# Performance work log

Hardware: AMD Instinct MI355X
Metric: run time of the kernel (lower is better)

The kernel has to match this reference:

```python
import jax, jax.numpy as jnp
import numpy as np

WS = 16; HEADS = 6; TOPK = 64; KIN = 128; EPS = 1e-10
B, C, H, W = 1, 192, 192, 192
HID = 4 * C  # mlp_ratio * dim


def _ln(x, g, b):
    m = jnp.mean(x, axis=-1, keepdims=True)
    v = jnp.var(x, axis=-1, keepdims=True)
    return (x - m) * jax.lax.rsqrt(v + 1e-5) * g + b


def _dw_gelu(x, hw, w, b):
    # depthwise 5x5 conv + exact GELU on token sequence (B, N, C)
    Bx, N, Cx = x.shape
    h, wd = hw
    xi = x.transpose(0, 2, 1).reshape(Bx, Cx, h, wd)
    y = jax.lax.conv_general_dilated(xi, w, (1, 1), 'SAME',
        feature_group_count=Cx, dimension_numbers=('NCHW', 'OIHW', 'NCHW'))
    y = jax.nn.gelu(y + b[None, :, None, None], approximate=False)
    return y.reshape(Bx, Cx, N).transpose(0, 2, 1)


def _window_partition(x):
    b, h, w, c = x.shape
    x = x.reshape(b, h // WS, WS, w // WS, WS, c)
    return x.transpose(0, 1, 3, 2, 4, 5).reshape(-1, WS * WS, c)


def _window_reverse(win, h, w):
    c = win.shape[-1]
    b = win.shape[0] // ((h // WS) * (w // WS))
    x = win.reshape(b, h // WS, w // WS, WS, WS, c)
    return x.transpose(0, 1, 3, 2, 4, 5).reshape(b, h, w, c)


def setup_inputs():
    key = jax.random.key(0)
    ks = jax.random.split(key, 16)
    b_, n = B * (H // WS) * (W // WS), WS * WS
    wgen = lambda k, sh: jax.random.normal(k, sh, jnp.float32) * 0.02
    p = {}
    p['features_mv'] = jax.random.normal(ks[0], (B, C, H, W), jnp.float32)
    p['pfa_values'] = jax.random.uniform(ks[1], (b_, HEADS, n, KIN), jnp.float32)
    p['pfa_indices'] = jax.random.randint(ks[2], (b_, HEADS, n, KIN), 0, n, jnp.int32)
    p['rpi'] = jax.random.randint(ks[3], (n, n), 0, (2 * WS - 1) ** 2, jnp.int32)
    p['ln1_g'] = jnp.ones((C,)); p['ln1_b'] = jnp.zeros((C,))
    p['Wq_w'] = wgen(ks[4], (C, C)); p['Wq_b'] = jnp.zeros((C,))
    p['Wk_w'] = wgen(ks[5], (C, C)); p['Wk_b'] = jnp.zeros((C,))
    p['Wv_w'] = wgen(ks[6], (C, C)); p['Wv_b'] = jnp.zeros((C,))
    p['lepe_w'] = wgen(ks[7], (C, 1, 5, 5)); p['lepe_b'] = jnp.zeros((C,))
    p['rpb_table'] = wgen(ks[8], ((2 * WS - 1) ** 2, HEADS))
    p['proj_w'] = wgen(ks[9], (C, C)); p['proj_b'] = jnp.zeros((C,))
    p['ln2_g'] = jnp.ones((C,)); p['ln2_b'] = jnp.zeros((C,))
    p['fc1_w'] = wgen(ks[10], (C, HID)); p['fc1_b'] = jnp.zeros((HID,))
    p['ffn_dw_w'] = wgen(ks[11], (HID, 1, 5, 5)); p['ffn_dw_b'] = jnp.zeros((HID,))
    p['fc2_w'] = wgen(ks[12], (HID, C)); p['fc2_b'] = jnp.zeros((C,))
    return p


def reference(features_mv, pfa_values, pfa_indices, rpi, ln1_g, ln1_b,
              Wq_w, Wq_b, Wk_w, Wk_b, Wv_w, Wv_b, lepe_w, lepe_b, rpb_table,
              proj_w, proj_b, ln2_g, ln2_b, fc1_w, fc1_b, ffn_dw_w, ffn_dw_b,
              fc2_w, fc2_b):
    b, c, h, w = features_mv.shape
    hd = c // HEADS
    x = features_mv.reshape(b, c, h * w).transpose(0, 2, 1)  # (B, HW, C)
    shortcut = x
    xn = _ln(x, ln1_g, ln1_b)
    q = xn @ Wq_w + Wq_b
    k = xn @ Wk_w + Wk_b
    v = xn @ Wv_w + Wv_b
    vl = _dw_gelu(v, (h, w), lepe_w, lepe_b)  # v_LePE
    qkvp = jnp.concatenate([q, k, v, vl], axis=-1).reshape(b, h, w, 4 * c)
    xw = _window_partition(qkvp)  # (b_, n, 4C)
    b_, n = xw.shape[0], WS * WS
    qkvp = xw.reshape(b_, n, 4, HEADS, hd).transpose(2, 0, 3, 1, 4)
    q, k, v, vl = qkvp[0] * hd ** -0.5, qkvp[1], qkvp[2], qkvp[3]
    # SMM_QmK: per-query gathered q.k — dense scores then index gather
    scores = jnp.einsum('bhid,bhjd->bhij', q, k)          # (b_, H, n, n)
    attn = jnp.take_along_axis(scores, pfa_indices, axis=-1)  # (b_, H, n, K)
    # relative position bias, gathered by the same sparse indices
    rpb = rpb_table[rpi.reshape(-1)].reshape(n, n, HEADS).transpose(2, 0, 1)
    rpb_g = jnp.take_along_axis(jnp.broadcast_to(rpb[None], (b_, HEADS, n, n)),
                                pfa_indices, axis=-1)
    attn = jax.nn.softmax(attn + rpb_g, axis=-1)
    # progressive focused attention: multiply by prior values, renormalize
    attn = attn * pfa_values
    attn = (attn + EPS) / (jnp.sum(attn, axis=-1, keepdims=True) + EPS)
    # in-layer top-k reselection (topk=64 < KIN=128)
    tv, ti = jax.lax.top_k(attn, TOPK)
    idx = jnp.take_along_axis(pfa_indices, ti, axis=-1)   # (b_, H, n, TOPK)
    # SMM_AmV: scatter sparse attn to dense (duplicates sum) then matmul
    BH = b_ * HEADS
    a = tv.reshape(BH, n, TOPK)
    idxf = idx.reshape(BH, n, TOPK)
    dense = jnp.zeros((BH, n, n), tv.dtype).at[
        jnp.arange(BH)[:, None, None], jnp.arange(n)[None, :, None], idxf].add(a)
    xo = jnp.einsum('bij,bjd->bid', dense, v.reshape(BH, n, hd))
    xo = xo.reshape(b_, HEADS, n, hd) + vl
    xo = xo.transpose(0, 2, 1, 3).reshape(b_, n, c) @ proj_w + proj_b
    xr = _window_reverse(xo.reshape(-1, WS, WS, c), h, w)
    x = shortcut + xr.reshape(b, h * w, c)
    # ConvFFN
    y = _ln(x, ln2_g, ln2_b) @ fc1_w + fc1_b
    y = jax.nn.gelu(y, approximate=False)
    y = y + _dw_gelu(y, (h, w), ffn_dw_w, ffn_dw_b)
    x = x + (y @ fc2_w + fc2_b)
    return x
```

## Files before the change

kernel.cpp:

```cpp
#include <hip/hip_runtime.h>
#include <math.h>

#define HW 36864
#define CD 192
#define NH 6
#define HDIM 32
#define HIDD 768

typedef unsigned short u16;
typedef __attribute__((ext_vector_type(8))) short bf16x8;
typedef __attribute__((ext_vector_type(4))) float f32x4;

__device__ __forceinline__ float gelu_f(float x) {
  return 0.5f * x * (1.0f + erff(x * 0.70710678118654752f));
}
__device__ __forceinline__ u16 f2b(float f) {
  union { float f; unsigned u; } v; v.f = f;
  unsigned r = v.u + 0x7fff + ((v.u >> 16) & 1);
  return (u16)(r >> 16);
}
__device__ __forceinline__ float b2f(u16 b) {
  union { unsigned u; float f; } v; v.u = ((unsigned)b) << 16;
  return v.f;
}
__device__ __forceinline__ float ldv(const float* p) { return *p; }
__device__ __forceinline__ float ldv(const u16* p) { return b2f(*p); }

__global__ __launch_bounds__(256)
void lnt_kernel(const float* __restrict__ in, const float* __restrict__ g,
                const float* __restrict__ b, u16* __restrict__ outTM)
{
  __shared__ float tile[64][193];
  __shared__ float red[64][8];
  __shared__ float2 stat2[64];
  __shared__ float gb[384];
  const int tid = threadIdx.x;
  const int part = tid >> 6, tk = tid & 63;
  const int tok = blockIdx.x * 64 + tk;
  if (tid < 192) { gb[tid] = g[tid]; gb[192 + tid] = b[tid]; }
  float s = 0.f, sq = 0.f;
  for (int c = part * 48; c < part * 48 + 48; ++c) {
    float v = in[(size_t)c * HW + tok];
    tile[tk][c] = v; s += v; sq += v * v;
  }
  red[tk][part] = s; red[tk][4 + part] = sq;
  __syncthreads();
  if (tid < 64) {
    float ss = red[tid][0] + red[tid][1] + red[tid][2] + red[tid][3];
    float qq = red[tid][4] + red[tid][5] + red[tid][6] + red[tid][7];
    float m = ss * (1.0f / CD);
    float var = fmaxf(qq * (1.0f / CD) - m * m, 0.f);
    stat2[tid] = make_float2(m, rsqrtf(var + 1e-5f));
  }
  __syncthreads();
  unsigned* op = (unsigned*)outTM + (size_t)blockIdx.x * 6144;
  #pragma unroll
  for (int r = 0; r < 24; ++r) {
    int idx = tid + r * 256;
    int tok2 = idx / 96, dc = idx - tok2 * 96;
    float2 st = stat2[tok2];
    int c = dc * 2;
    float v0 = (tile[tok2][c] - st.x) * st.y * gb[c] + gb[192 + c];
    float v1 = (tile[tok2][c + 1] - st.x) * st.y * gb[c + 1] + gb[192 + c + 1];
    op[idx] = (unsigned)f2b(v0) | ((unsigned)f2b(v1) << 16);
  }
}

__global__ __launch_bounds__(256)
void trans_kernel(const u16* __restrict__ in, u16* __restrict__ out, int C)
{
  __shared__ u16 ls[64][34];
  const int m0 = blockIdx.x * 64, c0 = blockIdx.y * 32;
  const int t = threadIdx.x;
  #pragma unroll
  for (int r = 0; r < 4; ++r) {
    int idx = t + r * 256;
    int c = idx >> 5, dm = idx & 31;
    unsigned d = *(const unsigned*)(in + (size_t)(c0 + c) * HW + m0 + dm * 2);
    ls[dm * 2][c] = (u16)d;
    ls[dm * 2 + 1][c] = (u16)(d >> 16);
  }
  __syncthreads();
  #pragma unroll
  for (int r = 0; r < 4; ++r) {
    int idx = t + r * 256;
    int m = idx >> 4, dc = idx & 15;
    unsigned d = (unsigned)ls[m][dc * 2] | ((unsigned)ls[m][dc * 2 + 1] << 16);
    *(unsigned*)(out + (size_t)(m0 + m) * C + c0 + dc * 2) = d;
  }
}

__global__ __launch_bounds__(256)
void wtrans_kernel(const float* __restrict__ in, u16* __restrict__ out, int K, int N)
{
  __shared__ float ls[32][33];
  const int k0 = blockIdx.x * 32, n0 = blockIdx.y * 32;
  const int t = threadIdx.x;
  #pragma unroll
  for (int r = 0; r < 4; ++r) {
    int idx = t + r * 256;
    int k = idx >> 5, n = idx & 31;
    ls[k][n] = in[(size_t)(k0 + k) * N + n0 + n];
  }
  __syncthreads();
  #pragma unroll
  for (int r = 0; r < 4; ++r) {
    int idx = t + r * 256;
    int n = idx >> 5, k = idx & 31;
    out[(size_t)(n0 + n) * K + k0 + k] = f2b(ls[k][n]);
  }
}

__global__ __launch_bounds__(256)
void wtrans4_kernel(const float* __restrict__ w0, const float* __restrict__ w1,
                    const float* __restrict__ w2, const float* __restrict__ w3,
                    u16* __restrict__ out)
{
  __shared__ float ls[32][33];
  const int z = blockIdx.z;
  const float* in = (z == 0) ? w0 : (z == 1 ? w1 : (z == 2 ? w2 : w3));
  u16* op = out + (size_t)z * CD * CD;
  const int k0 = blockIdx.x * 32, n0 = blockIdx.y * 32;
  const int t = threadIdx.x;
  #pragma unroll
  for (int r = 0; r < 4; ++r) {
    int idx = t + r * 256;
    int k = idx >> 5, n = idx & 31;
    ls[k][n] = in[(size_t)(k0 + k) * CD + n0 + n];
  }
  __syncthreads();
  #pragma unroll
  for (int r = 0; r < 4; ++r) {
    int idx = t + r * 256;
    int n = idx >> 5, k = idx & 31;
    op[(size_t)(n0 + n) * CD + k0 + k] = f2b(ls[k][n]);
  }
}

template<int MODE>
__global__ __launch_bounds__(256, 4)
void mgemm_kernel(const u16* __restrict__ A,
                  const u16* __restrict__ W0, const u16* __restrict__ W1, const u16* __restrict__ W2,
                  const float* __restrict__ b0, const float* __restrict__ b1, const float* __restrict__ b2,
                  const float* __restrict__ aux, void* __restrict__ outv,
                  int K, int segN)
{
  const int n0 = blockIdx.x * 64;
  const int m0 = blockIdx.y * 128;
  const int seg = n0 / segN;
  const u16* Wp = (seg == 0) ? W0 : (seg == 1 ? W1 : W2);
  const float* biasp = (seg == 0) ? b0 : (seg == 1 ? b1 : b2);
  const int nl0 = n0 - seg * segN;

  __shared__ u16 As[128 * 32];
  __shared__ u16 Bs[64 * 32];

  const int tid = threadIdx.x;
  const int lane = tid & 63, wave = tid >> 6;
  const int wm = (wave >> 1) * 64, wn = (wave & 1) * 32;
  const int fm = lane & 15, fq = lane >> 4;
  const int ar = tid >> 2, akq = tid & 3;

  f32x4 acc[4][2];
  #pragma unroll
  for (int i = 0; i < 4; ++i) { acc[i][0] = (f32x4)(0.f); acc[i][1] = (f32x4)(0.f); }

  uint4 rA0, rA1, rB, nA0, nA1, nB;
  rA0 = *(const uint4*)(A + (size_t)(m0 + ar) * K + akq * 8);
  rA1 = *(const uint4*)(A + (size_t)(m0 + ar + 64) * K + akq * 8);
  rB  = *(const uint4*)(Wp + (size_t)(nl0 + ar) * K + akq * 8);

  for (int k0 = 0; k0 < K; k0 += 32) {
    *(uint4*)(&As[ar * 32 + akq * 8]) = rA0;
    *(uint4*)(&As[(ar + 64) * 32 + akq * 8]) = rA1;
    *(uint4*)(&Bs[ar * 32 + akq * 8]) = rB;
    __syncthreads();
    const int kn = (k0 + 32 < K) ? k0 + 32 : k0;
    nA0 = *(const uint4*)(A + (size_t)(m0 + ar) * K + kn + akq * 8);
    nA1 = *(const uint4*)(A + (size_t)(m0 + ar + 64) * K + kn + akq * 8);
    nB  = *(const uint4*)(Wp + (size_t)(nl0 + ar) * K + kn + akq * 8);
    bf16x8 af[4], bf[2];
    #pragma unroll
    for (int mt = 0; mt < 4; ++mt)
      af[mt] = *(const bf16x8*)(&As[(wm + mt * 16 + fm) * 32 + fq * 8]);
    #pragma unroll
    for (int nt = 0; nt < 2; ++nt)
      bf[nt] = *(const bf16x8*)(&Bs[(wn + nt * 16 + fm) * 32 + fq * 8]);
    #pragma unroll
    for (int mt = 0; mt < 4; ++mt)
      #pragma unroll
      for (int nt = 0; nt < 2; ++nt)
        acc[mt][nt] = __builtin_amdgcn_mfma_f32_16x16x32_bf16(af[mt], bf[nt], acc[mt][nt], 0, 0, 0);
    __syncthreads();
    rA0 = nA0; rA1 = nA1; rB = nB;
  }

  #pragma unroll
  for (int nt = 0; nt < 2; ++nt) {
    const int n = n0 + wn + nt * 16 + fm;
    const float bia = biasp[nl0 + wn + nt * 16 + fm];
    #pragma unroll
    for (int mt = 0; mt < 4; ++mt) {
      const int mb = m0 + wm + mt * 16 + fq * 4;
      float o[4];
      #pragma unroll
      for (int r = 0; r < 4; ++r) o[r] = acc[mt][nt][r] + bia;
      if (MODE == 0) {
        const float sc = (seg == 0) ? 0.17677669529663689f : 1.0f;
        u16 h0 = f2b(o[0] * sc), h1 = f2b(o[1] * sc), h2 = f2b(o[2] * sc), h3 = f2b(o[3] * sc);
        uint2 pk = make_uint2((unsigned)h0 | ((unsigned)h1 << 16), (unsigned)h2 | ((unsigned)h3 << 16));
        *(uint2*)((u16*)outv + (size_t)n * HW + mb) = pk;
      } else if (MODE == 1) {
        const float4 ax = *(const float4*)(aux + (size_t)n * HW + mb);
        *(float4*)((float*)outv + (size_t)n * HW + mb) =
            make_float4(o[0] + ax.x, o[1] + ax.y, o[2] + ax.z, o[3] + ax.w);
      } else if (MODE == 2) {
        u16 h0 = f2b(gelu_f(o[0])), h1 = f2b(gelu_f(o[1]));
        u16 h2 = f2b(gelu_f(o[2])), h3 = f2b(gelu_f(o[3]));
        uint2 pk = make_uint2((unsigned)h0 | ((unsigned)h1 << 16), (unsigned)h2 | ((unsigned)h3 << 16));
        *(uint2*)((u16*)outv + (size_t)n * HW + mb) = pk;
      } else {
        const float4 ax = *(const float4*)(aux + (size_t)n * HW + mb);
        float* op = (float*)outv;
        op[(size_t)(mb + 0) * CD + n] = o[0] + ax.x;
        op[(size_t)(mb + 1) * CD + n] = o[1] + ax.y;
        op[(size_t)(mb + 2) * CD + n] = o[2] + ax.z;
        op[(size_t)(mb + 3) * CD + n] = o[3] + ax.w;
      }
    }
  }
}

template<bool ADD>
__global__ __launch_bounds__(256)
void dwconv_kernel(const u16* __restrict__ in, const float* __restrict__ w,
                   const float* __restrict__ bias, u16* __restrict__ out)
{
  const int plane = blockIdx.z;
  const int bx = blockIdx.x * 64, by = blockIdx.y * 4;
  __shared__ float tile[8][68];
  __shared__ float ws[26];
  const int tid = threadIdx.x;
  if (tid < 26) ws[tid] = (tid < 25) ? w[plane * 25 + tid] : bias[plane];
  const u16* ip = in + (size_t)plane * HW;
  for (int e = tid; e < 544; e += 256) {
    int r = e / 68, cc = e - r * 68;
    int gy = by + r - 2, gx = bx + cc - 2;
    tile[r][cc] = (gy >= 0 && gy < 192 && gx >= 0 && gx < 192) ? b2f(ip[gy * 192 + gx]) : 0.f;
  }
  __syncthreads();
  const int tx = tid & 63, ty = tid >> 6;
  float acc = 0.f;
  #pragma unroll
  for (int dy = 0; dy < 5; ++dy)
    #pragma unroll
    for (int dx = 0; dx < 5; ++dx)
      acc = fmaf(tile[ty + dy][tx + dx], ws[dy * 5 + dx], acc);
  float v = gelu_f(acc + ws[25]);
  if (ADD) v += tile[ty + 2][tx + 2];
  out[(size_t)plane * HW + (by + ty) * 192 + bx + tx] = f2b(v);
}

__global__ __launch_bounds__(512, 4)
void attn_kernel(const u16* __restrict__ qg, const u16* __restrict__ kg,
                 const u16* __restrict__ vg, const u16* __restrict__ vlg,
                 const float* __restrict__ pfa_v, const int* __restrict__ pfa_i,
                 const int* __restrict__ rpi, const float* __restrict__ rpb_t,
                 u16* __restrict__ attn_out)
{
  const int h = blockIdx.x;
  const int win = blockIdx.y;
  const int wy = (win / 12) * 16;
  const int wx = (win - (win / 12) * 12) * 16;
  const size_t hb = (size_t)h * HDIM * HW;

  __shared__ u16 kT[256][40];
  __shared__ u16 vT[32][258];
  __shared__ float Sb[32][264];
  __shared__ u16 qT[32][40];
  __shared__ float rpb_h[964];
  __shared__ float2 selbuf[8][64];

  const int tid = threadIdx.x;
  const int lane = tid & 63, wave = tid >> 6;

  for (int r = tid; r < 961; r += 512) rpb_h[r] = rpb_t[r * 6 + h];

  #pragma unroll
  for (int r = 0; r < 8; ++r) {
    int idx = tid + r * 512;
    int d = idx >> 7, jp = idx & 127, j = jp * 2;
    int pg = (wy + (j >> 4)) * 192 + (wx + (j & 15));
    ushort2 kv = *(const ushort2*)(kg + hb + (size_t)d * HW + pg);
    kT[j][d] = kv.x; kT[j + 1][d] = kv.y;
    *(ushort2*)&vT[d][j] = *(const ushort2*)(vg + hb + (size_t)d * HW + pg);
  }
  __syncthreads();

  const size_t wb = ((size_t)win * NH + h) * 256;

  for (int pass = 0; pass < 8; ++pass) {
    {
      int d = tid >> 4, ip = tid & 15, i = pass * 32 + ip * 2;
      int pg = (wy + (i >> 4)) * 192 + (wx + (i & 15));
      ushort2 qv = *(const ushort2*)(qg + hb + (size_t)d * HW + pg);
      qT[ip * 2][d] = qv.x; qT[ip * 2 + 1][d] = qv.y;
    }
    __syncthreads();
    {
      const int it = wave & 1;
      bf16x8 aq = *(const bf16x8*)&qT[it * 16 + (lane & 15)][(lane >> 4) * 8];
      #pragma unroll
      for (int t = 0; t < 4; ++t) {
        int j0 = ((wave >> 1) * 4 + t) * 16;
        bf16x8 bk = *(const bf16x8*)&kT[j0 + (lane & 15)][(lane >> 4) * 8];
        f32x4 c = __builtin_amdgcn_mfma_f32_16x16x32_bf16(aq, bk, (f32x4)(0.f), 0, 0, 0);
        const int col = j0 + (lane & 15), rowb = it * 16 + (lane >> 4) * 4;
        Sb[rowb + 0][col] = c[0]; Sb[rowb + 1][col] = c[1];
        Sb[rowb + 2][col] = c[2]; Sb[rowb + 3][col] = c[3];
      }
    }
    __syncthreads();
    int pj1[4], pj2[4]; float pv1[4], pv2[4], rb1[4], rb2[4];
    #pragma unroll
    for (int u = 0; u < 4; ++u) {
      const int i = pass * 32 + u * 8 + wave;
      const size_t base = (wb + (size_t)i) * 128;
      pj1[u] = pfa_i[base + lane];  pj2[u] = pfa_i[base + 64 + lane];
      pv1[u] = pfa_v[base + lane];  pv2[u] = pfa_v[base + 64 + lane];
    }
    #pragma unroll
    for (int u = 0; u < 4; ++u) {
      const int i = pass * 32 + u * 8 + wave;
      rb1[u] = rpb_h[rpi[i * 256 + pj1[u]]];
      rb2[u] = rpb_h[rpi[i * 256 + pj2[u]]];
    }
    #pragma unroll
    for (int u = 0; u < 4; ++u) {
      const int iq = u * 8 + wave;
      const int i  = pass * 32 + iq;
      const int j1 = pj1[u], j2 = pj2[u];
      float s1 = Sb[iq][j1] + rb1[u];
      float s2 = Sb[iq][j2] + rb2[u];
      float mx = fmaxf(s1, s2);
      #pragma unroll
      for (int o = 32; o > 0; o >>= 1) mx = fmaxf(mx, __shfl_xor(mx, o));
      float e1 = expf(s1 - mx), e2 = expf(s2 - mx);
      float sA = e1 + e2;
      float sB = e1 * pv1[u] + e2 * pv2[u];
      #pragma unroll
      for (int o = 32; o > 0; o >>= 1) { sA += __shfl_xor(sA, o); sB += __shfl_xor(sB, o); }
      const float rs = 1.0f / sA;
      float a1 = e1 * rs * pv1[u];
      float a2 = e2 * rs * pv2[u];
      const float rden = 1.0f / (sB * rs + 1e-10f);
      a1 = (a1 + 1e-10f) * rden;
      a2 = (a2 + 1e-10f) * rden;
      const unsigned ub1 = __float_as_uint(a1), ub2 = __float_as_uint(a2);
      unsigned thr = 0u;
      for (int bit = 30; bit >= 0; --bit) {
        unsigned cand = thr | (1u << bit);
        int cnt = (int)__popcll(__ballot(ub1 >= cand)) + (int)__popcll(__ballot(ub2 >= cand));
        if (cnt >= 64) { thr = cand; if (cnt == 64) break; }
      }
      const unsigned long long lmlt = (1ull << lane) - 1ull;
      const bool gt1 = ub1 > thr, gt2 = ub2 > thr;
      const bool eq1 = ub1 == thr, eq2 = ub2 == thr;
      const unsigned long long meq1 = __ballot(eq1), meq2 = __ballot(eq2);
      const int need = 64 - (int)__popcll(__ballot(gt1)) - (int)__popcll(__ballot(gt2));
      const bool sel1 = gt1 || (eq1 && (int)__popcll(meq1 & lmlt) < need);
      const bool sel2 = gt2 || (eq2 && ((int)__popcll(meq1) + (int)__popcll(meq2 & lmlt)) < need);
      const unsigned long long ms1 = __ballot(sel1), ms2 = __ballot(sel2);
      const int pos1 = (int)__popcll(ms1 & lmlt);
      const int pos2 = (int)__popcll(ms1) + (int)__popcll(ms2 & lmlt);
      if (sel1) selbuf[wave][pos1] = make_float2(a1, __int_as_float(j1));
      if (sel2) selbuf[wave][pos2] = make_float2(a2, __int_as_float(j2));
      const int d = lane & 31, half = lane >> 5;
      float acc = 0.f;
      #pragma unroll
      for (int c = 0; c < 4; ++c) {
        float2 sv[8];
        #pragma unroll
        for (int q4 = 0; q4 < 4; ++q4)
          *(float4*)&sv[q4 * 2] = *(const float4*)&selbuf[wave][half * 32 + c * 8 + q4 * 2];
        #pragma unroll
        for (int s = 0; s < 8; ++s)
          acc = fmaf(sv[s].x, b2f(vT[d][__float_as_int(sv[s].y)]), acc);
      }
      acc += __shfl_xor(acc, 32);
      const int pg = (wy + (i >> 4)) * 192 + (wx + (i & 15));
      if (lane < 32) {
        float o = acc + b2f(vlg[hb + (size_t)d * HW + pg]);
        attn_out[(size_t)pg * CD + h * HDIM + d] = f2b(o);
      }
    }
    __syncthreads();
  }
}

extern "C" void kernel_launch(void* const* d_in, const int* in_sizes, int n_in,
                              void* d_out, int out_size, void* d_ws, size_t ws_size,
                              hipStream_t stream)
{
  (void)in_sizes; (void)n_in; (void)out_size; (void)ws_size;
  const float* features = (const float*)d_in[0];
  const float* pfa_v    = (const float*)d_in[1];
  const int*   pfa_i    = (const int*)d_in[2];
  const int*   rpi      = (const int*)d_in[3];
  const float* ln1_g    = (const float*)d_in[4];
  const float* ln1_b    = (const float*)d_in[5];
  const float* Wq_w     = (const float*)d_in[6];
  const float* Wq_b     = (const float*)d_in[7];
  const float* Wk_w     = (const float*)d_in[8];
  const float* Wk_b     = (const float*)d_in[9];
  const float* Wv_w     = (const float*)d_in[10];
  const float* Wv_b     = (const float*)d_in[11];
  const float* lepe_w   = (const float*)d_in[12];
  const float* lepe_b   = (const float*)d_in[13];
  const float* rpb_t    = (const float*)d_in[14];
  const float* proj_w   = (const float*)d_in[15];
  const float* proj_b   = (const float*)d_in[16];
  const float* ln2_g    = (const float*)d_in[17];
  const float* ln2_b    = (const float*)d_in[18];
  const float* fc1_w    = (const float*)d_in[19];
  const float* fc1_b    = (const float*)d_in[20];
  const float* dw_w     = (const float*)d_in[21];
  const float* dw_b     = (const float*)d_in[22];
  const float* fc2_w    = (const float*)d_in[23];
  const float* fc2_b    = (const float*)d_in[24];

  char* ws = (char*)d_ws;
  const size_t S  = (size_t)HW * CD;
  const size_t SB = S * 4;
  u16*   xnt    = (u16*)(ws);
  u16*   qkvb   = (u16*)(ws + SB / 2);
  u16*   q_ = qkvb; u16* k_ = qkvb + S; u16* v_ = qkvb + 2 * S;
  u16*   vl     = (u16*)(ws + 2 * SB);
  u16*   attn_o = (u16*)(ws + 2 * SB + SB / 2);
  float* x2     = (float*)(ws + 3 * SB);
  u16*   xn2t   = (u16*)(ws + 4 * SB);
  u16*   y_     = (u16*)(ws + 4 * SB + SB / 2);
  u16*   y2_    = (u16*)(ws + 6 * SB + SB / 2);
  u16*   y2t    = (u16*)(ws);
  u16*   wqt  = (u16*)(ws + 8 * SB + SB / 2);
  u16*   wkt  = wqt + 36864;
  u16*   wvt  = wkt + 36864;
  u16*   wpt  = wvt + 36864;
  u16*   wf1t = wpt + 36864;
  u16*   wf2t = wf1t + 147456;
  float* out = (float*)d_out;

  wtrans4_kernel<<<dim3(6, 6, 4), 256, 0, stream>>>(Wq_w, Wk_w, Wv_w, proj_w, wqt);
  wtrans_kernel<<<dim3(6, 24), 256, 0, stream>>>(fc1_w, wf1t, 192, 768);
  wtrans_kernel<<<dim3(24, 6), 256, 0, stream>>>(fc2_w, wf2t, 768, 192);
  lnt_kernel<<<dim3(HW / 64), 256, 0, stream>>>(features, ln1_g, ln1_b, xnt);
  mgemm_kernel<0><<<dim3(9, HW / 128), 256, 0, stream>>>(xnt, wqt, wkt, wvt, Wq_b, Wk_b, Wv_b,
                                                         nullptr, qkvb, 192, 192);
  dwconv_kernel<false><<<dim3(3, 48, 192), 256, 0, stream>>>(v_, lepe_w, lepe_b, vl);
  attn_kernel<<<dim3(6, 144), 512, 0, stream>>>(q_, k_, v_, vl, pfa_v, pfa_i, rpi, rpb_t, attn_o);
  mgemm_kernel<1><<<dim3(3, HW / 128), 256, 0, stream>>>(attn_o, wpt, wpt, wpt, proj_b, proj_b, proj_b,
                                                         features, x2, 192, 1 << 30);
  lnt_kernel<<<dim3(HW / 64), 256, 0, stream>>>(x2, ln2_g, ln2_b, xn2t);
  mgemm_kernel<2><<<dim3(12, HW / 128), 256, 0, stream>>>(xn2t, wf1t, wf1t, wf1t, fc1_b, fc1_b, fc1_b,
                                                          nullptr, y_, 192, 1 << 30);
  dwconv_kernel<true><<<dim3(3, 48, 768), 256, 0, stream>>>(y_, dw_w, dw_b, y2_);
  trans_kernel<<<dim3(HW / 64, 24), 256, 0, stream>>>(y2_, y2t, HIDD);
  mgemm_kernel<3><<<dim3(3, HW / 128), 256, 0, stream>>>(y2t, wf2t, wf2t, wf2t, fc2_b, fc2_b, fc2_b,
                                                         x2, out, 768, 1 << 30);
}
```

Before: 800.7 us.

## Fuse dwconv with transpose, precompute dense RPB, pad GEMM LDS, simplify attention normalization

The depthwise conv kernel now processes 32 channels per block and writes token-major output directly, so the separate transpose kernel goes away and the attention reads LEPE token-major. A new kernel expands the relative position bias into a dense per-head 256x256 table once. The attention adds that bias straight after the MFMA instead of doing gathered rpi lookups, and moves the softmax/renormalisation algebra after top-k so fewer values are rescaled. GEMM shared-memory tiles are padded from 32 to 40 columns to reduce bank conflicts. The cost is an extra 1.5 MB bias table read per window-head and a larger LDS footprint in the conv kernel.

```diff
diff --git a/kernel.cpp b/kernel.cpp
--- a/kernel.cpp
+++ b/kernel.cpp
@@ -23,8 +23,12 @@
   union { unsigned u; float f; } v; v.u = ((unsigned)b) << 16;
   return v.f;
 }
-__device__ __forceinline__ float ldv(const float* p) { return *p; }
-__device__ __forceinline__ float ldv(const u16* p) { return b2f(*p); }
+__device__ __forceinline__ float b2f_lo(unsigned u) {
+  union { unsigned x; float f; } v; v.x = u << 16; return v.f;
+}
+__device__ __forceinline__ float b2f_hi(unsigned u) {
+  union { unsigned x; float f; } v; v.x = u & 0xffff0000u; return v.f;
+}
 
 __global__ __launch_bounds__(256)
 void lnt_kernel(const float* __restrict__ in, const float* __restrict__ g,
@@ -67,30 +71,6 @@
 }
 
 __global__ __launch_bounds__(256)
-void trans_kernel(const u16* __restrict__ in, u16* __restrict__ out, int C)
-{
-  __shared__ u16 ls[64][34];
-  const int m0 = blockIdx.x * 64, c0 = blockIdx.y * 32;
-  const int t = threadIdx.x;
-  #pragma unroll
-  for (int r = 0; r < 4; ++r) {
-    int idx = t + r * 256;
-    int c = idx >> 5, dm = idx & 31;
-    unsigned d = *(const unsigned*)(in + (size_t)(c0 + c) * HW + m0 + dm * 2);
-    ls[dm * 2][c] = (u16)d;
-    ls[dm * 2 + 1][c] = (u16)(d >> 16);
-  }
-  __syncthreads();
-  #pragma unroll
-  for (int r = 0; r < 4; ++r) {
-    int idx = t + r * 256;
-    int m = idx >> 4, dc = idx & 15;
-    unsigned d = (unsigned)ls[m][dc * 2] | ((unsigned)ls[m][dc * 2 + 1] << 16);
-    *(unsigned*)(out + (size_t)(m0 + m) * C + c0 + dc * 2) = d;
-  }
-}
-
-__global__ __launch_bounds__(256)
 void wtrans_kernel(const float* __restrict__ in, u16* __restrict__ out, int K, int N)
 {
   __shared__ float ls[32][33];
@@ -135,6 +115,17 @@
     int n = idx >> 5, k = idx & 31;
     op[(size_t)(n0 + n) * CD + k0 + k] = f2b(ls[k][n]);
   }
+}
+
+__global__ __launch_bounds__(256)
+void rpbg_kernel(const int* __restrict__ rpi, const float* __restrict__ rpb_t,
+                 float* __restrict__ out)
+{
+  const int i = blockIdx.x, j = threadIdx.x;
+  const int r = rpi[i * 256 + j];
+  #pragma unroll
+  for (int h = 0; h < NH; ++h)
+    out[(size_t)h * 65536 + i * 256 + j] = rpb_t[r * NH + h];
 }
 
 template<int MODE>
@@ -152,8 +143,8 @@
   const float* biasp = (seg == 0) ? b0 : (seg == 1 ? b1 : b2);
   const int nl0 = n0 - seg * segN;
 
-  __shared__ u16 As[128 * 32];
-  __shared__ u16 Bs[64 * 32];
+  __shared__ u16 As[128 * 40];
+  __shared__ u16 Bs[64 * 40];
 
   const int tid = threadIdx.x;
   const int lane = tid & 63, wave = tid >> 6;
@@ -171,9 +162,9 @@
   rB  = *(const uint4*)(Wp + (size_t)(nl0 + ar) * K + akq * 8);
 
   for (int k0 = 0; k0 < K; k0 += 32) {
-    *(uint4*)(&As[ar * 32 + akq * 8]) = rA0;
-    *(uint4*)(&As[(ar + 64) * 32 + akq * 8]) = rA1;
-    *(uint4*)(&Bs[ar * 32 + akq * 8]) = rB;
+    *(uint4*)(&As[ar * 40 + akq * 8]) = rA0;
+    *(uint4*)(&As[(ar + 64) * 40 + akq * 8]) = rA1;
+    *(uint4*)(&Bs[ar * 40 + akq * 8]) = rB;
     __syncthreads();
     const int kn = (k0 + 32 < K) ? k0 + 32 : k0;
     nA0 = *(const uint4*)(A + (size_t)(m0 + ar) * K + kn + akq * 8);
@@ -182,10 +173,10 @@
     bf16x8 af[4], bf[2];
     #pragma unroll
     for (int mt = 0; mt < 4; ++mt)
-      af[mt] = *(const bf16x8*)(&As[(wm + mt * 16 + fm) * 32 + fq * 8]);
+      af[mt] = *(const bf16x8*)(&As[(wm + mt * 16 + fm) * 40 + fq * 8]);
     #pragma unroll
     for (int nt = 0; nt < 2; ++nt)
-      bf[nt] = *(const bf16x8*)(&Bs[(wn + nt * 16 + fm) * 32 + fq * 8]);
+      bf[nt] = *(const bf16x8*)(&Bs[(wn + nt * 16 + fm) * 40 + fq * 8]);
     #pragma unroll
     for (int mt = 0; mt < 4; ++mt)
       #pragma unroll
@@ -233,40 +224,82 @@
 
 template<bool ADD>
 __global__ __launch_bounds__(256)
-void dwconv_kernel(const u16* __restrict__ in, const float* __restrict__ w,
-                   const float* __restrict__ bias, u16* __restrict__ out)
-{
-  const int plane = blockIdx.z;
+void dwconv_tm_kernel(const u16* __restrict__ in, const float* __restrict__ w,
+                      const float* __restrict__ bias, u16* __restrict__ out, int PL)
+{
+  const int p0 = blockIdx.z * 32;
   const int bx = blockIdx.x * 64, by = blockIdx.y * 4;
-  __shared__ float tile[8][68];
-  __shared__ float ws[26];
+  __shared__ u16 tile[32 * 546];
+  __shared__ float ws[32][26];
   const int tid = threadIdx.x;
-  if (tid < 26) ws[tid] = (tid < 25) ? w[plane * 25 + tid] : bias[plane];
-  const u16* ip = in + (size_t)plane * HW;
-  for (int e = tid; e < 544; e += 256) {
-    int r = e / 68, cc = e - r * 68;
-    int gy = by + r - 2, gx = bx + cc - 2;
-    tile[r][cc] = (gy >= 0 && gy < 192 && gx >= 0 && gx < 192) ? b2f(ip[gy * 192 + gx]) : 0.f;
-  }
-  __syncthreads();
-  const int tx = tid & 63, ty = tid >> 6;
-  float acc = 0.f;
-  #pragma unroll
-  for (int dy = 0; dy < 5; ++dy)
-    #pragma unroll
-    for (int dx = 0; dx < 5; ++dx)
-      acc = fmaf(tile[ty + dy][tx + dx], ws[dy * 5 + dx], acc);
-  float v = gelu_f(acc + ws[25]);
-  if (ADD) v += tile[ty + 2][tx + 2];
-  out[(size_t)plane * HW + (by + ty) * 192 + bx + tx] = f2b(v);
+  for (int e = tid; e < 832; e += 256) {
+    int p = e / 26, q = e - p * 26;
+    ws[p][q] = (q < 25) ? w[(p0 + p) * 25 + q] : bias[p0 + p];
+  }
+  for (int e = tid; e < 256 * 34; e += 256) {
+    int rp = e / 34, ch = e - rp * 34;
+    int p = rp >> 3, r = rp & 7;
+    int gy = by + r - 2, gx = bx + ch * 2 - 2;
+    unsigned val = 0;
+    if (gy >= 0 && gy < 192 && gx >= 0 && gx < 192)
+      val = *(const unsigned*)(in + (size_t)(p0 + p) * HW + gy * 192 + gx);
+    *(unsigned*)&tile[p * 546 + r * 68 + ch * 2] = val;
+  }
+  __syncthreads();
+  const int txp = tid >> 3, pg = tid & 7;
+  u16 res[4][2][4];
+  #pragma unroll
+  for (int pp = 0; pp < 4; ++pp) {
+    const int p = pg * 4 + pp;
+    const u16* tp = &tile[p * 546];
+    float o0[4] = {0.f, 0.f, 0.f, 0.f}, o1[4] = {0.f, 0.f, 0.f, 0.f};
+    #pragma unroll
+    for (int ir = 0; ir < 8; ++ir) {
+      const unsigned* rowp = (const unsigned*)(tp + ir * 68 + txp * 2);
+      unsigned ua = rowp[0], ub = rowp[1], uc = rowp[2];
+      float f0 = b2f_lo(ua), f1 = b2f_hi(ua), f2 = b2f_lo(ub);
+      float f3 = b2f_hi(ub), f4 = b2f_lo(uc), f5 = b2f_hi(uc);
+      #pragma unroll
+      for (int dy = 0; dy < 5; ++dy) {
+        const int r = ir - dy;
+        if (r >= 0 && r < 4) {
+          const float w0 = ws[p][dy * 5 + 0], w1 = ws[p][dy * 5 + 1], w2 = ws[p][dy * 5 + 2];
+          const float w3 = ws[p][dy * 5 + 3], w4 = ws[p][dy * 5 + 4];
+          o0[r] += f0 * w0 + f1 * w1 + f2 * w2 + f3 * w3 + f4 * w4;
+          o1[r] += f1 * w0 + f2 * w1 + f3 * w2 + f4 * w3 + f5 * w4;
+        }
+      }
+    }
+    const float bb = ws[p][25];
+    #pragma unroll
+    for (int r = 0; r < 4; ++r) {
+      float v0 = gelu_f(o0[r] + bb);
+      float v1 = gelu_f(o1[r] + bb);
+      if (ADD) {
+        unsigned ctr = *(const unsigned*)(tp + (r + 2) * 68 + txp * 2 + 2);
+        v0 += b2f_lo(ctr); v1 += b2f_hi(ctr);
+      }
+      res[pp][0][r] = f2b(v0); res[pp][1][r] = f2b(v1);
+    }
+  }
+  #pragma unroll
+  for (int r = 0; r < 4; ++r) {
+    #pragma unroll
+    for (int c = 0; c < 2; ++c) {
+      const int pix = (by + r) * 192 + bx + txp * 2 + c;
+      uint2 pk = make_uint2(
+        (unsigned)res[0][c][r] | ((unsigned)res[1][c][r] << 16),
+        (unsigned)res[2][c][r] | ((unsigned)res[3][c][r] << 16));
+      *(uint2*)(out + (size_t)pix * PL + p0 + pg * 4) = pk;
+    }
+  }
 }
 
 __global__ __launch_bounds__(512, 4)
 void attn_kernel(const u16* __restrict__ qg, const u16* __restrict__ kg,
-                 const u16* __restrict__ vg, const u16* __restrict__ vlg,
+                 const u16* __restrict__ vg, const u16* __restrict__ vlt,
                  const float* __restrict__ pfa_v, const int* __restrict__ pfa_i,
-                 const int* __restrict__ rpi, const float* __restrict__ rpb_t,
-                 u16* __restrict__ attn_out)
+                 const float* __restrict__ rpbg, u16* __restrict__ attn_out)
 {
   const int h = blockIdx.x;
   const int win = blockIdx.y;
@@ -274,17 +307,14 @@
   const int wx = (win - (win / 12) * 12) * 16;
   const size_t hb = (size_t)h * HDIM * HW;
 
-  __shared__ u16 kT[256][40];
-  __shared__ u16 vT[32][258];
-  __shared__ float Sb[32][264];
-  __shared__ u16 qT[32][40];
-  __shared__ float rpb_h[964];
+  __shared__ u16 kT[256 * 40];
+  __shared__ u16 vJ[256 * 40];
+  __shared__ float Sb[32 * 260];
+  __shared__ u16 qT[32 * 40];
   __shared__ float2 selbuf[8][64];
 
   const int tid = threadIdx.x;
   const int lane = tid & 63, wave = tid >> 6;
-
-  for (int r = tid; r < 961; r += 512) rpb_h[r] = rpb_t[r * 6 + h];
 
   #pragma unroll
   for (int r = 0; r < 8; ++r) {
@@ -292,36 +322,44 @@
     int d = idx >> 7, jp = idx & 127, j = jp * 2;
     int pg = (wy + (j >> 4)) * 192 + (wx + (j & 15));
     ushort2 kv = *(const ushort2*)(kg + hb + (size_t)d * HW + pg);
-    kT[j][d] = kv.x; kT[j + 1][d] = kv.y;
-    *(ushort2*)&vT[d][j] = *(const ushort2*)(vg + hb + (size_t)d * HW + pg);
+    kT[j * 40 + d] = kv.x; kT[(j + 1) * 40 + d] = kv.y;
+    ushort2 vv = *(const ushort2*)(vg + hb + (size_t)d * HW + pg);
+    vJ[j * 40 + d] = vv.x; vJ[(j + 1) * 40 + d] = vv.y;
   }
   __syncthreads();
 
   const size_t wb = ((size_t)win * NH + h) * 256;
+  const float* rpp = rpbg + (size_t)h * 65536;
 
   for (int pass = 0; pass < 8; ++pass) {
     {
       int d = tid >> 4, ip = tid & 15, i = pass * 32 + ip * 2;
       int pg = (wy + (i >> 4)) * 192 + (wx + (i & 15));
       ushort2 qv = *(const ushort2*)(qg + hb + (size_t)d * HW + pg);
-      qT[ip * 2][d] = qv.x; qT[ip * 2 + 1][d] = qv.y;
+      qT[(ip * 2) * 40 + d] = qv.x; qT[(ip * 2 + 1) * 40 + d] = qv.y;
     }
     __syncthreads();
     {
       const int it = wave & 1;
-      bf16x8 aq = *(const bf16x8*)&qT[it * 16 + (lane & 15)][(lane >> 4) * 8];
+      const int fm = lane & 15, fq = lane >> 4;
+      bf16x8 aq = *(const bf16x8*)&qT[(it * 16 + fm) * 40 + fq * 8];
       #pragma unroll
       for (int t = 0; t < 4; ++t) {
         int j0 = ((wave >> 1) * 4 + t) * 16;
-        bf16x8 bk = *(const bf16x8*)&kT[j0 + (lane & 15)][(lane >> 4) * 8];
+        bf16x8 bk = *(const bf16x8*)&kT[(j0 + fm) * 40 + fq * 8];
         f32x4 c = __builtin_amdgcn_mfma_f32_16x16x32_bf16(aq, bk, (f32x4)(0.f), 0, 0, 0);
-        const int col = j0 + (lane & 15), rowb = it * 16 + (lane >> 4) * 4;
-        Sb[rowb + 0][col] = c[0]; Sb[rowb + 1][col] = c[1];
-        Sb[rowb + 2][col] = c[2]; Sb[rowb + 3][col] = c[3];
+        const int col = j0 + fm, rowb = it * 16 + fq * 4;
+        const int ib = pass * 32 + rowb;
+        c[0] += rpp[(size_t)(ib + 0) * 256 + col];
+        c[1] += rpp[(size_t)(ib + 1) * 256 + col];
+        c[2] += rpp[(size_t)(ib + 2) * 256 + col];
+        c[3] += rpp[(size_t)(ib + 3) * 256 + col];
+        Sb[(rowb + 0) * 260 + col] = c[0]; Sb[(rowb + 1) * 260 + col] = c[1];
+        Sb[(rowb + 2) * 260 + col] = c[2]; Sb[(rowb + 3) * 260 + col] = c[3];
       }
     }
     __syncthreads();
-    int pj1[4], pj2[4]; float pv1[4], pv2[4], rb1[4], rb2[4];
+    int pj1[4], pj2[4]; float pv1[4], pv2[4];
     #pragma unroll
     for (int u = 0; u < 4; ++u) {
       const int i = pass * 32 + u * 8 + wave;
@@ -331,38 +369,26 @@
     }
     #pragma unroll
     for (int u = 0; u < 4; ++u) {
-      const int i = pass * 32 + u * 8 + wave;
-      rb1[u] = rpb_h[rpi[i * 256 + pj1[u]]];
-      rb2[u] = rpb_h[rpi[i * 256 + pj2[u]]];
-    }
-    #pragma unroll
-    for (int u = 0; u < 4; ++u) {
       const int iq = u * 8 + wave;
       const int i  = pass * 32 + iq;
       const int j1 = pj1[u], j2 = pj2[u];
-      float s1 = Sb[iq][j1] + rb1[u];
-      float s2 = Sb[iq][j2] + rb2[u];
+      float s1 = Sb[iq * 260 + j1];
+      float s2 = Sb[iq * 260 + j2];
       float mx = fmaxf(s1, s2);
       #pragma unroll
       for (int o = 32; o > 0; o >>= 1) mx = fmaxf(mx, __shfl_xor(mx, o));
       float e1 = expf(s1 - mx), e2 = expf(s2 - mx);
-      float sA = e1 + e2;
-      float sB = e1 * pv1[u] + e2 * pv2[u];
-      #pragma unroll
-      for (int o = 32; o > 0; o >>= 1) { sA += __shfl_xor(sA, o); sB += __shfl_xor(sB, o); }
-      const float rs = 1.0f / sA;
-      float a1 = e1 * rs * pv1[u];
-      float a2 = e2 * rs * pv2[u];
-      const float rden = 1.0f / (sB * rs + 1e-10f);
-      a1 = (a1 + 1e-10f) * rden;
-      a2 = (a2 + 1e-10f) * rden;
-      const unsigned ub1 = __float_as_uint(a1), ub2 = __float_as_uint(a2);
+      float u1 = e1 * pv1[u], u2 = e2 * pv2[u];
+      const unsigned ub1 = __float_as_uint(u1), ub2 = __float_as_uint(u2);
       unsigned thr = 0u;
       for (int bit = 30; bit >= 0; --bit) {
         unsigned cand = thr | (1u << bit);
         int cnt = (int)__popcll(__ballot(ub1 >= cand)) + (int)__popcll(__ballot(ub2 >= cand));
         if (cnt >= 64) { thr = cand; if (cnt == 64) break; }
       }
+      float sA = e1 + e2, sB = u1 + u2;
+      #pragma unroll
+      for (int o = 32; o > 0; o >>= 1) { sA += __shfl_xor(sA, o); sB += __shfl_xor(sB, o); }
       const unsigned long long lmlt = (1ull << lane) - 1ull;
       const bool gt1 = ub1 > thr, gt2 = ub2 > thr;
       const bool eq1 = ub1 == thr, eq2 = ub2 == thr;
@@ -373,8 +399,10 @@
       const unsigned long long ms1 = __ballot(sel1), ms2 = __ballot(sel2);
       const int pos1 = (int)__popcll(ms1 & lmlt);
       const int pos2 = (int)__popcll(ms1) + (int)__popcll(ms2 & lmlt);
-      if (sel1) selbuf[wave][pos1] = make_float2(a1, __int_as_float(j1));
-      if (sel2) selbuf[wave][pos2] = make_float2(a2, __int_as_float(j2));
+      const float t = 1e-10f * sA;
+      const float rden = 1.0f / (sB + t);
+      if (sel1) selbuf[wave][pos1] = make_float2((u1 + t) * rden, __int_as_float(j1));
+      if (sel2) selbuf[wave][pos2] = make_float2((u2 + t) * rden, __int_as_float(j2));
       const int d = lane & 31, half = lane >> 5;
       float acc = 0.f;
       #pragma unroll
@@ -385,12 +413,12 @@
           *(float4*)&sv[q4 * 2] = *(const float4*)&selbuf[wave][half * 32 + c * 8 + q4 * 2];
         #pragma unroll
         for (int s = 0; s < 8; ++s)
-          acc = fmaf(sv[s].x, b2f(vT[d][__float_as_int(sv[s].y)]), acc);
+          acc = fmaf(sv[s].x, b2f(vJ[__float_as_int(sv[s].y) * 40 + d]), acc);
       }
       acc += __shfl_xor(acc, 32);
       const int pg = (wy + (i >> 4)) * 192 + (wx + (i & 15));
       if (lane < 32) {
-        float o = acc + b2f(vlg[hb + (size_t)d * HW + pg]);
+        float o = acc + b2f(vlt[(size_t)pg * CD + h * HDIM + d]);
         attn_out[(size_t)pg * CD + h * HDIM + d] = f2b(o);
       }
     }
@@ -435,36 +463,36 @@
   u16*   xnt    = (u16*)(ws);
   u16*   qkvb   = (u16*)(ws + SB / 2);
   u16*   q_ = qkvb; u16* k_ = qkvb + S; u16* v_ = qkvb + 2 * S;
-  u16*   vl     = (u16*)(ws + 2 * SB);
+  u16*   vlt    = (u16*)(ws + 2 * SB);
   u16*   attn_o = (u16*)(ws + 2 * SB + SB / 2);
   float* x2     = (float*)(ws + 3 * SB);
   u16*   xn2t   = (u16*)(ws + 4 * SB);
   u16*   y_     = (u16*)(ws + 4 * SB + SB / 2);
-  u16*   y2_    = (u16*)(ws + 6 * SB + SB / 2);
-  u16*   y2t    = (u16*)(ws);
+  u16*   y2t    = (u16*)(ws + 6 * SB + SB / 2);
   u16*   wqt  = (u16*)(ws + 8 * SB + SB / 2);
   u16*   wkt  = wqt + 36864;
   u16*   wvt  = wkt + 36864;
   u16*   wpt  = wvt + 36864;
   u16*   wf1t = wpt + 36864;
   u16*   wf2t = wf1t + 147456;
+  float* rpbg = (float*)(wf2t + 147456 + 128);
   float* out = (float*)d_out;
 
   wtrans4_kernel<<<dim3(6, 6, 4), 256, 0, stream>>>(Wq_w, Wk_w, Wv_w, proj_w, wqt);
   wtrans_kernel<<<dim3(6, 24), 256, 0, stream>>>(fc1_w, wf1t, 192, 768);
   wtrans_kernel<<<dim3(24, 6), 256, 0, stream>>>(fc2_w, wf2t, 768, 192);
+  rpbg_kernel<<<dim3(256), 256, 0, stream>>>(rpi, rpb_t, rpbg);
   lnt_kernel<<<dim3(HW / 64), 256, 0, stream>>>(features, ln1_g, ln1_b, xnt);
   mgemm_kernel<0><<<dim3(9, HW / 128), 256, 0, stream>>>(xnt, wqt, wkt, wvt, Wq_b, Wk_b, Wv_b,
                                                          nullptr, qkvb, 192, 192);
-  dwconv_kernel<false><<<dim3(3, 48, 192), 256, 0, stream>>>(v_, lepe_w, lepe_b, vl);
-  attn_kernel<<<dim3(6, 144), 512, 0, stream>>>(q_, k_, v_, vl, pfa_v, pfa_i, rpi, rpb_t, attn_o);
+  dwconv_tm_kernel<false><<<dim3(3, 48, 6), 256, 0, stream>>>(v_, lepe_w, lepe_b, vlt, CD);
+  attn_kernel<<<dim3(6, 144), 512, 0, stream>>>(q_, k_, v_, vlt, pfa_v, pfa_i, rpbg, attn_o);
   mgemm_kernel<1><<<dim3(3, HW / 128), 256, 0, stream>>>(attn_o, wpt, wpt, wpt, proj_b, proj_b, proj_b,
                                                          features, x2, 192, 1 << 30);
   lnt_kernel<<<dim3(HW / 64), 256, 0, stream>>>(x2, ln2_g, ln2_b, xn2t);
   mgemm_kernel<2><<<dim3(12, HW / 128), 256, 0, stream>>>(xn2t, wf1t, wf1t, wf1t, fc1_b, fc1_b, fc1_b,
                                                           nullptr, y_, 192, 1 << 30);
-  dwconv_kernel<true><<<dim3(3, 48, 768), 256, 0, stream>>>(y_, dw_w, dw_b, y2_);
-  trans_kernel<<<dim3(HW / 64, 24), 256, 0, stream>>>(y2_, y2t, HIDD);
+  dwconv_tm_kernel<true><<<dim3(3, 48, 24), 256, 0, stream>>>(y_, dw_w, dw_b, y2t, HIDD);
   mgemm_kernel<3><<<dim3(3, HW / 128), 256, 0, stream>>>(y2t, wf2t, wf2t, wf2t, fc2_b, fc2_b, fc2_b,
                                                          x2, out, 768, 1 << 30);
 }
```

After: 800.7 us. Within noise of the previous version (+0.0%).
